# Optimization experiments

Measured on AMD Instinct MI355X. Metric: run time of the kernel, lower is better.

Reference implementation:

```python
import jax, jax.numpy as jnp
import numpy as np

N = 100000   # nodes
E = 500000   # edges
NS = 64      # scalar (0e) multiplicity
NV = 32      # vector (1o) multiplicity
DIM = NS + 3 * NV  # 160
AVG_NEI = 5.0
INV_SQRT3 = 0.5773502691896258


def setup_inputs() -> dict:
    key = jax.random.key(0)
    ks = jax.random.split(key, 14)
    return {
        "node_feats": jax.random.normal(ks[0], (N, DIM), jnp.float32),
        "node_attrs": jax.random.normal(ks[1], (N, 4), jnp.float32),
        "edge_message": jax.random.normal(ks[2], (E, DIM), jnp.float32),
        "edge_index": jax.random.randint(ks[3], (2, E), 0, N, dtype=jnp.int32),
        # UVU tensor product internal shared weights (one weight per u channel per path)
        "w_tp_00": jax.random.normal(ks[4], (NS,), jnp.float32),  # 0e x 0e -> 0e
        "w_tp_01": jax.random.normal(ks[5], (NS,), jnp.float32),  # 0e x 1o -> 1o
        "w_tp_10": jax.random.normal(ks[6], (NV,), jnp.float32),  # 1o x 0e -> 1o
        "w_tp_11": jax.random.normal(ks[7], (NV,), jnp.float32),  # 1o x 1o -> 0e
        # irreps Linear: tp out has 96x0e + 96x1o -> 96x0e + 32x1o
        "W_lin_s": jax.random.normal(ks[8], (NS + NV, NS + NV), jnp.float32),
        "W_lin_v": jax.random.normal(ks[9], (NS + NV, NV), jnp.float32),
        # FullyConnectedTensorProduct self-connection (uvw, v=1)
        "W_sc_000": jax.random.normal(ks[10], (NS, NS + NV), jnp.float32),
        "W_sc_110": jax.random.normal(ks[11], (NV, NS + NV), jnp.float32),
        "W_sc_011": jax.random.normal(ks[12], (NS, NV), jnp.float32),
        "W_sc_101": jax.random.normal(ks[13], (NV, NV), jnp.float32),
    }


def reference(node_feats, node_attrs, edge_message, edge_index,
              w_tp_00, w_tp_01, w_tp_10, w_tp_11,
              W_lin_s, W_lin_v, W_sc_000, W_sc_110, W_sc_011, W_sc_101):
    edge_dst = edge_index[1]
    # scatter-aggregate edge messages per destination node
    msg = jax.ops.segment_sum(edge_message, edge_dst, num_segments=N)
    msg = msg / jnp.sqrt(AVG_NEI)

    ms = msg[:, :NS]                         # [N, 64] scalars
    mv = msg[:, NS:].reshape(N, NV, 3)       # [N, 32, 3] vectors
    a_s = node_attrs[:, :1]                  # [N, 1]
    a_v = node_attrs[:, 1:]                  # [N, 3]

    # UVU tensor product (msg x attrs), per-channel shared weights
    s00 = ms * a_s * w_tp_00                                            # [N,64] 0e
    s11 = jnp.einsum('nuc,nc->nu', mv, a_v) * INV_SQRT3 * w_tp_11       # [N,32] 0e
    v01 = ms[:, :, None] * a_v[:, None, :] * w_tp_01[None, :, None]     # [N,64,3] 1o
    v10 = mv * a_s[:, :, None] * w_tp_10[None, :, None]                 # [N,32,3] 1o
    tp_s = jnp.concatenate([s00, s11], axis=1)   # [N,96]
    tp_v = jnp.concatenate([v01, v10], axis=1)   # [N,96,3]

    # irreps Linear (block diagonal per l, fan-in normalized)
    inv_fan = 1.0 / jnp.sqrt(jnp.float32(NS + NV))
    lin_s = (tp_s @ W_lin_s) * inv_fan                              # [N,96]
    lin_v = jnp.einsum('nuc,uw->nwc', tp_v, W_lin_v) * inv_fan      # [N,32,3]

    # self-connection: FullyConnectedTensorProduct(node_feats_in, node_attrs)
    xs = node_feats[:, :NS]
    xv = node_feats[:, NS:].reshape(N, NV, 3)
    inv2 = 1.0 / jnp.sqrt(2.0)
    sc_s = ((xs * a_s) @ W_sc_000 / jnp.sqrt(jnp.float32(NS))
            + (jnp.einsum('nuc,nc->nu', xv, a_v) * INV_SQRT3) @ W_sc_110 / jnp.sqrt(jnp.float32(NV))) * inv2
    sc_v = (jnp.einsum('nu,uw,nc->nwc', xs, W_sc_011, a_v) / jnp.sqrt(jnp.float32(NS))
            + jnp.einsum('nuc,uw->nwc', xv * a_s[:, :, None], W_sc_101) / jnp.sqrt(jnp.float32(NV))) * inv2

    h_s = lin_s + sc_s   # [N,96] = 64 scalars + 32 gates
    h_v = lin_v + sc_v   # [N,32,3]

    # gated activation: silu on scalars, sigmoid gates scale the vectors
    out_s = jax.nn.silu(h_s[:, :NS])
    gates = jax.nn.sigmoid(h_s[:, NS:])
    out_v = gates[:, :, None] * h_v
    return jnp.concatenate([out_s, out_v.reshape(N, NV * 3)], axis=1)  # [N,160]
```

## Files before the change

kernel.cpp:

```cpp
#include <hip/hip_runtime.h>

typedef unsigned short u16;
typedef unsigned int u32;

#define Nn 100000
#define Ee 500000
#define DIM 160
#define CAP 48

__device__ __forceinline__ float bf2f(u16 u) {
    return __uint_as_float(((u32)u) << 16);
}
__device__ __forceinline__ u16 f2bf(float f) {
    u32 i = __float_as_uint(f);
    return (u16)((i + 0x7FFFu + ((i >> 16) & 1u)) >> 16);
}

__global__ __launch_bounds__(256) void hist_fill_k(const int* __restrict__ ei,
                                                   int* __restrict__ cnt,
                                                   int* __restrict__ bucket) {
    int e = blockIdx.x * 256 + threadIdx.x;
    if (e >= Ee) return;
    int dst = ei[Ee + e];
    int pos = atomicAdd(&cnt[dst], 1);
    if (pos < CAP) bucket[(size_t)dst * CAP + pos] = e;
}

__global__ __launch_bounds__(256) void gather_tr_k(const float* __restrict__ em,
                                                   const int* __restrict__ bucket,
                                                   const int* __restrict__ cnt,
                                                   u16* __restrict__ msgT) {
    __shared__ u16 tile[160][66];
    int n0 = blockIdx.x * 64;
    int w = threadIdx.x >> 6;
    int lane = threadIdx.x & 63;
    const float s = 0.4472135954999579f;

    for (int i = 0; i < 16; ++i) {
        int n = n0 + w * 16 + i;
        float a0 = 0.f, a1 = 0.f, a2 = 0.f;
        if (n < Nn) {
            int deg = cnt[n];
            if (deg > CAP) deg = CAP;
            const int* base = bucket + (size_t)n * CAP;
            for (int k = 0; k < deg; ++k) {
                int e = base[k];
                const float* r = em + (size_t)e * DIM;
                a0 += r[lane];
                a1 += r[64 + lane];
                if (lane < 32) a2 += r[128 + lane];
            }
        }
        int col = w * 16 + i;
        tile[lane][col] = f2bf(a0 * s);
        tile[64 + lane][col] = f2bf(a1 * s);
        if (lane < 32) tile[128 + lane][col] = f2bf(a2 * s);
    }
    __syncthreads();
    for (int k = 0; k < 40; ++k) {
        int d = w * 40 + k;
        int n = n0 + lane;
        if (n < Nn) msgT[(size_t)d * Nn + n] = tile[d][lane];
    }
}

__global__ void transpose_f2b_k(const float* __restrict__ in, u16* __restrict__ outp) {
    __shared__ float t[32][33];
    int r0 = blockIdx.x * 32, c0 = blockIdx.y * 32;
    int tx = threadIdx.x, ty = threadIdx.y;
    t[ty][tx] = in[(size_t)(r0 + ty) * DIM + c0 + tx];
    __syncthreads();
    outp[(size_t)(c0 + ty) * Nn + r0 + tx] = f2bf(t[tx][ty]);
}

__global__ __launch_bounds__(256) void prep_weights_k(
    const float* __restrict__ Wls, const float* __restrict__ Wlv,
    const float* __restrict__ W000, const float* __restrict__ W110,
    const float* __restrict__ W011, const float* __restrict__ W101,
    const float* __restrict__ w00, const float* __restrict__ w01,
    const float* __restrict__ w10, const float* __restrict__ w11,
    float* __restrict__ W) {
    int i = blockIdx.x * 256 + threadIdx.x;
    const float inv_fan = 0.10206207261596577f;
    const float IS3 = 0.5773502691896258f;
    if (i < 9216) {
        int u = i / 96;
        float sc = inv_fan * (u < 64 ? w00[u] : IS3 * w11[u - 64]);
        W[i] = Wls[i] * sc;
    } else if (i < 12288) {
        int j = i - 9216; int u = j / 32;
        float sc = inv_fan * (u < 64 ? w01[u] : w10[u - 64]);
        W[i] = Wlv[j] * sc;
    } else if (i < 18432) {
        W[i] = W000[i - 12288] * 0.08838834764831845f;
    } else if (i < 21504) {
        W[i] = W110[i - 18432] * (0.125f * IS3);
    } else if (i < 23552) {
        W[i] = W011[i - 21504] * 0.08838834764831845f;
    } else {
        W[i] = W101[i - 23552] * 0.125f;
    }
}

__global__ __launch_bounds__(256) void node_s_k(
    const u16* __restrict__ msgT, const u16* __restrict__ featsT,
    const float* __restrict__ attrs, const float* __restrict__ W,
    float* __restrict__ out, float* __restrict__ gbuf) {
    __shared__ float st[256][33];
    int wb = blockIdx.y;
    int n0 = blockIdx.x * 256;
    int t = threadIdx.x;
    int n = n0 + t;
    bool active = (n < Nn);
    int nc = active ? n : (Nn - 1);

    const float* Wls  = W;
    const float* W000 = W + 12288;
    const float* W110 = W + 18432;

    float4 a = *reinterpret_cast<const float4*>(attrs + (size_t)nc * 4);
    float a_s = a.x, av0 = a.y, av1 = a.z, av2 = a.w;

    float accU[32], accJ[32];
    #pragma unroll
    for (int w = 0; w < 32; ++w) { accU[w] = 0.f; accJ[w] = 0.f; }

    const float* R1 = Wls + wb * 32;
    const float* R2 = W000 + wb * 32;
    const float* R3 = W110 + wb * 32;

    for (int u = 0; u < 64; ++u) {
        float m = bf2f(msgT[(size_t)u * Nn + nc]);
        float x = bf2f(featsT[(size_t)u * Nn + nc]);
        const float* r1 = R1 + u * 96;
        const float* r2 = R2 + u * 96;
        #pragma unroll
        for (int w = 0; w < 32; ++w) accU[w] += m * r1[w] + x * r2[w];
    }
    for (int j = 0; j < 32; ++j) {
        size_t d = (size_t)(64 + 3 * j) * Nn + nc;
        float dv = bf2f(msgT[d]) * av0 + bf2f(msgT[d + Nn]) * av1
                 + bf2f(msgT[d + 2 * Nn]) * av2;
        float dx = bf2f(featsT[d]) * av0 + bf2f(featsT[d + Nn]) * av1
                 + bf2f(featsT[d + 2 * Nn]) * av2;
        const float* r1 = R1 + (64 + j) * 96;
        const float* r2 = R3 + j * 96;
        #pragma unroll
        for (int w = 0; w < 32; ++w) accJ[w] += dv * r1[w] + dx * r2[w];
    }

    if (wb < 2) {
        #pragma unroll
        for (int w = 0; w < 32; ++w) {
            float h = a_s * accU[w] + accJ[w];
            st[t][w] = h / (1.f + __expf(-h));
        }
        __syncthreads();
        int off = wb * 32;
        for (int k = 0; k < 32; ++k) {
            int f = k * 256 + t;
            int node = f >> 5, w = f & 31;
            int n2 = n0 + node;
            if (n2 < Nn) out[(size_t)n2 * DIM + off + w] = st[node][w];
        }
    } else {
        #pragma unroll
        for (int w = 0; w < 32; ++w) {
            float h = a_s * accU[w] + accJ[w];
            if (active) gbuf[(size_t)w * Nn + n] = 1.f / (1.f + __expf(-h));
        }
    }
}

__global__ __launch_bounds__(256) void node_v_k(
    const u16* __restrict__ msgT, const u16* __restrict__ featsT,
    const float* __restrict__ attrs, const float* __restrict__ W,
    const float* __restrict__ gbuf, float* __restrict__ out) {
    __shared__ float st[256][49];
    int half = blockIdx.y;
    int w0 = half * 16;
    int n0 = blockIdx.x * 256;
    int t = threadIdx.x;
    int n = n0 + t;
    bool active = (n < Nn);
    int nc = active ? n : (Nn - 1);

    const float* Wlv  = W + 9216;
    const float* W011 = W + 21504;
    const float* W101 = W + 23552;

    float4 a = *reinterpret_cast<const float4*>(attrs + (size_t)nc * 4);
    float a_s = a.x;
    float av[3] = {a.y, a.z, a.w};

    float ss[16];
    #pragma unroll
    for (int w = 0; w < 16; ++w) ss[w] = 0.f;
    for (int u = 0; u < 64; ++u) {
        float m = bf2f(msgT[(size_t)u * Nn + nc]);
        float x = bf2f(featsT[(size_t)u * Nn + nc]);
        const float* r1 = Wlv + u * 32 + w0;
        const float* r2 = W011 + u * 32 + w0;
        #pragma unroll
        for (int w = 0; w < 16; ++w) ss[w] += m * r1[w] + x * r2[w];
    }

    float hj[16][3];
    #pragma unroll
    for (int w = 0; w < 16; ++w) {
        hj[w][0] = 0.f; hj[w][1] = 0.f; hj[w][2] = 0.f;
    }
    for (int j = 0; j < 32; ++j) {
        size_t d = (size_t)(64 + 3 * j) * Nn + nc;
        float m0 = bf2f(msgT[d]), m1 = bf2f(msgT[d + Nn]), m2 = bf2f(msgT[d + 2 * Nn]);
        float x0 = bf2f(featsT[d]), x1 = bf2f(featsT[d + Nn]), x2 = bf2f(featsT[d + 2 * Nn]);
        const float* r1 = Wlv + (64 + j) * 32 + w0;
        const float* r2 = W101 + j * 32 + w0;
        #pragma unroll
        for (int w = 0; w < 16; ++w) {
            float wv = r1[w], wx = r2[w];
            hj[w][0] += m0 * wv + x0 * wx;
            hj[w][1] += m1 * wv + x1 * wx;
            hj[w][2] += m2 * wv + x2 * wx;
        }
    }

    #pragma unroll
    for (int w = 0; w < 16; ++w) {
        float g = gbuf[(size_t)(w0 + w) * Nn + nc];
        #pragma unroll
        for (int c = 0; c < 3; ++c) {
            float hv = av[c] * ss[w] + a_s * hj[w][c];
            st[t][w * 3 + c] = g * hv;
        }
    }
    __syncthreads();
    int off = 64 + w0 * 3;
    for (int k = 0; k < 48; ++k) {
        int f = k * 256 + t;
        int node = f / 48;
        int idx = f - node * 48;
        int n2 = n0 + node;
        if (n2 < Nn) out[(size_t)n2 * DIM + off + idx] = st[node][idx];
    }
}

extern "C" void kernel_launch(void* const* d_in, const int* in_sizes, int n_in,
                              void* d_out, int out_size, void* d_ws, size_t ws_size,
                              hipStream_t stream) {
    const float* feats = (const float*)d_in[0];
    const float* attrs = (const float*)d_in[1];
    const float* em    = (const float*)d_in[2];
    const int*   ei    = (const int*)d_in[3];
    const float* w00   = (const float*)d_in[4];
    const float* w01   = (const float*)d_in[5];
    const float* w10   = (const float*)d_in[6];
    const float* w11   = (const float*)d_in[7];
    const float* Wls   = (const float*)d_in[8];
    const float* Wlv   = (const float*)d_in[9];
    const float* W000  = (const float*)d_in[10];
    const float* W110  = (const float*)d_in[11];
    const float* W011  = (const float*)d_in[12];
    const float* W101  = (const float*)d_in[13];

    char* ws = (char*)d_ws;
    int*   bucket = (int*)  (ws);
    int*   cnt    = (int*)  (ws + 19200000);
    u16*   msgT   = (u16*)  (ws + 19600000);
    u16*   featsT = (u16*)  (ws + 51600000);
    float* gbuf   = (float*)(ws + 83600000);
    float* W      = (float*)(ws + 96400000);

    hipMemsetAsync(cnt, 0, Nn * sizeof(int), stream);

    hist_fill_k<<<(Ee + 255) / 256, 256, 0, stream>>>(ei, cnt, bucket);

    gather_tr_k<<<(Nn + 63) / 64, 256, 0, stream>>>(em, bucket, cnt, msgT);

    dim3 tb(32, 32);
    transpose_f2b_k<<<dim3(Nn / 32, DIM / 32), tb, 0, stream>>>(feats, featsT);

    prep_weights_k<<<96, 256, 0, stream>>>(Wls, Wlv, W000, W110, W011, W101,
                                           w00, w01, w10, w11, W);

    node_s_k<<<dim3((Nn + 255) / 256, 3), 256, 0, stream>>>(msgT, featsT, attrs, W,
                                                            (float*)d_out, gbuf);

    node_v_k<<<dim3((Nn + 255) / 256, 2), 256, 0, stream>>>(msgT, featsT, attrs, W,
                                                            gbuf, (float*)d_out);
}
```

Before: 782.3 us.

## Fuse feats transpose into gather kernel and pack msg/feat bf16 pairs

Drops the separate node-feature transpose kernel and folds its work into the edge-gather kernel. That kernel now writes one interleaved u32 array holding the bf16 message in the high half and the bf16 feature in the low half. The node kernels then issue a single 32-bit load per channel instead of two 16-bit loads, and unpack with shifts and masks. The gather block grows to 512 threads with 8 nodes per wave, and 32-bit index arithmetic replaces size_t, at the cost of higher shared memory use per block.

```diff
diff --git a/kernel.cpp b/kernel.cpp
--- a/kernel.cpp
+++ b/kernel.cpp
@@ -8,9 +8,6 @@
 #define DIM 160
 #define CAP 48
 
-__device__ __forceinline__ float bf2f(u16 u) {
-    return __uint_as_float(((u32)u) << 16);
-}
 __device__ __forceinline__ u16 f2bf(float f) {
     u32 i = __float_as_uint(f);
     return (u16)((i + 0x7FFFu + ((i >> 16) & 1u)) >> 16);
@@ -26,19 +23,22 @@
     if (pos < CAP) bucket[(size_t)dst * CAP + pos] = e;
 }
 
-__global__ __launch_bounds__(256) void gather_tr_k(const float* __restrict__ em,
+__global__ __launch_bounds__(512) void gather_tr_k(const float* __restrict__ em,
+                                                   const float* __restrict__ feats,
                                                    const int* __restrict__ bucket,
                                                    const int* __restrict__ cnt,
-                                                   u16* __restrict__ msgT) {
-    __shared__ u16 tile[160][66];
+                                                   u32* __restrict__ mfT) {
+    __shared__ u32 tile[160][66];
     int n0 = blockIdx.x * 64;
     int w = threadIdx.x >> 6;
     int lane = threadIdx.x & 63;
     const float s = 0.4472135954999579f;
 
-    for (int i = 0; i < 16; ++i) {
-        int n = n0 + w * 16 + i;
+    for (int i = 0; i < 8; ++i) {
+        int col = w * 8 + i;
+        int n = n0 + col;
         float a0 = 0.f, a1 = 0.f, a2 = 0.f;
+        float f0 = 0.f, f1 = 0.f, f2 = 0.f;
         if (n < Nn) {
             int deg = cnt[n];
             if (deg > CAP) deg = CAP;
@@ -50,27 +50,24 @@
                 a1 += r[64 + lane];
                 if (lane < 32) a2 += r[128 + lane];
             }
-        }
-        int col = w * 16 + i;
-        tile[lane][col] = f2bf(a0 * s);
-        tile[64 + lane][col] = f2bf(a1 * s);
-        if (lane < 32) tile[128 + lane][col] = f2bf(a2 * s);
+            const float* f = feats + (size_t)n * DIM;
+            f0 = f[lane];
+            f1 = f[64 + lane];
+            if (lane < 32) f2 = f[128 + lane];
+        }
+        tile[lane][col]      = ((u32)f2bf(a0 * s) << 16) | f2bf(f0);
+        tile[64 + lane][col] = ((u32)f2bf(a1 * s) << 16) | f2bf(f1);
+        if (lane < 32)
+            tile[128 + lane][col] = ((u32)f2bf(a2 * s) << 16) | f2bf(f2);
     }
     __syncthreads();
-    for (int k = 0; k < 40; ++k) {
-        int d = w * 40 + k;
-        int n = n0 + lane;
-        if (n < Nn) msgT[(size_t)d * Nn + n] = tile[d][lane];
-    }
-}
-
-__global__ void transpose_f2b_k(const float* __restrict__ in, u16* __restrict__ outp) {
-    __shared__ float t[32][33];
-    int r0 = blockIdx.x * 32, c0 = blockIdx.y * 32;
-    int tx = threadIdx.x, ty = threadIdx.y;
-    t[ty][tx] = in[(size_t)(r0 + ty) * DIM + c0 + tx];
-    __syncthreads();
-    outp[(size_t)(c0 + ty) * Nn + r0 + tx] = f2bf(t[tx][ty]);
+    int n = n0 + lane;
+    if (n < Nn) {
+        for (int k = 0; k < 20; ++k) {
+            int d = w * 20 + k;
+            mfT[d * Nn + n] = tile[d][lane];
+        }
+    }
 }
 
 __global__ __launch_bounds__(256) void prep_weights_k(
@@ -102,10 +99,13 @@
     }
 }
 
+__device__ __forceinline__ float hi_f(u32 v) { return __uint_as_float(v & 0xFFFF0000u); }
+__device__ __forceinline__ float lo_f(u32 v) { return __uint_as_float(v << 16); }
+
 __global__ __launch_bounds__(256) void node_s_k(
-    const u16* __restrict__ msgT, const u16* __restrict__ featsT,
-    const float* __restrict__ attrs, const float* __restrict__ W,
-    float* __restrict__ out, float* __restrict__ gbuf) {
+    const u32* __restrict__ mfT, const float* __restrict__ attrs,
+    const float* __restrict__ W, float* __restrict__ out,
+    float* __restrict__ gbuf) {
     __shared__ float st[256][33];
     int wb = blockIdx.y;
     int n0 = blockIdx.x * 256;
@@ -130,19 +130,19 @@
     const float* R3 = W110 + wb * 32;
 
     for (int u = 0; u < 64; ++u) {
-        float m = bf2f(msgT[(size_t)u * Nn + nc]);
-        float x = bf2f(featsT[(size_t)u * Nn + nc]);
+        u32 v = mfT[u * Nn + nc];
+        float m = hi_f(v);
+        float x = lo_f(v);
         const float* r1 = R1 + u * 96;
         const float* r2 = R2 + u * 96;
         #pragma unroll
         for (int w = 0; w < 32; ++w) accU[w] += m * r1[w] + x * r2[w];
     }
     for (int j = 0; j < 32; ++j) {
-        size_t d = (size_t)(64 + 3 * j) * Nn + nc;
-        float dv = bf2f(msgT[d]) * av0 + bf2f(msgT[d + Nn]) * av1
-                 + bf2f(msgT[d + 2 * Nn]) * av2;
-        float dx = bf2f(featsT[d]) * av0 + bf2f(featsT[d + Nn]) * av1
-                 + bf2f(featsT[d + 2 * Nn]) * av2;
+        int d = (64 + 3 * j) * Nn + nc;
+        u32 v0 = mfT[d], v1 = mfT[d + Nn], v2 = mfT[d + 2 * Nn];
+        float dv = hi_f(v0) * av0 + hi_f(v1) * av1 + hi_f(v2) * av2;
+        float dx = lo_f(v0) * av0 + lo_f(v1) * av1 + lo_f(v2) * av2;
         const float* r1 = R1 + (64 + j) * 96;
         const float* r2 = R3 + j * 96;
         #pragma unroll
@@ -167,15 +167,15 @@
         #pragma unroll
         for (int w = 0; w < 32; ++w) {
             float h = a_s * accU[w] + accJ[w];
-            if (active) gbuf[(size_t)w * Nn + n] = 1.f / (1.f + __expf(-h));
+            if (active) gbuf[w * Nn + n] = 1.f / (1.f + __expf(-h));
         }
     }
 }
 
 __global__ __launch_bounds__(256) void node_v_k(
-    const u16* __restrict__ msgT, const u16* __restrict__ featsT,
-    const float* __restrict__ attrs, const float* __restrict__ W,
-    const float* __restrict__ gbuf, float* __restrict__ out) {
+    const u32* __restrict__ mfT, const float* __restrict__ attrs,
+    const float* __restrict__ W, const float* __restrict__ gbuf,
+    float* __restrict__ out) {
     __shared__ float st[256][49];
     int half = blockIdx.y;
     int w0 = half * 16;
@@ -197,8 +197,9 @@
     #pragma unroll
     for (int w = 0; w < 16; ++w) ss[w] = 0.f;
     for (int u = 0; u < 64; ++u) {
-        float m = bf2f(msgT[(size_t)u * Nn + nc]);
-        float x = bf2f(featsT[(size_t)u * Nn + nc]);
+        u32 v = mfT[u * Nn + nc];
+        float m = hi_f(v);
+        float x = lo_f(v);
         const float* r1 = Wlv + u * 32 + w0;
         const float* r2 = W011 + u * 32 + w0;
         #pragma unroll
@@ -211,9 +212,10 @@
         hj[w][0] = 0.f; hj[w][1] = 0.f; hj[w][2] = 0.f;
     }
     for (int j = 0; j < 32; ++j) {
-        size_t d = (size_t)(64 + 3 * j) * Nn + nc;
-        float m0 = bf2f(msgT[d]), m1 = bf2f(msgT[d + Nn]), m2 = bf2f(msgT[d + 2 * Nn]);
-        float x0 = bf2f(featsT[d]), x1 = bf2f(featsT[d + Nn]), x2 = bf2f(featsT[d + 2 * Nn]);
+        int d = (64 + 3 * j) * Nn + nc;
+        u32 v0 = mfT[d], v1 = mfT[d + Nn], v2 = mfT[d + 2 * Nn];
+        float m0 = hi_f(v0), m1 = hi_f(v1), m2 = hi_f(v2);
+        float x0 = lo_f(v0), x1 = lo_f(v1), x2 = lo_f(v2);
         const float* r1 = Wlv + (64 + j) * 32 + w0;
         const float* r2 = W101 + j * 32 + w0;
         #pragma unroll
@@ -227,7 +229,7 @@
 
     #pragma unroll
     for (int w = 0; w < 16; ++w) {
-        float g = gbuf[(size_t)(w0 + w) * Nn + nc];
+        float g = gbuf[(w0 + w) * Nn + nc];
         #pragma unroll
         for (int c = 0; c < 3; ++c) {
             float hv = av[c] * ss[w] + a_s * hj[w][c];
@@ -266,8 +268,7 @@
     char* ws = (char*)d_ws;
     int*   bucket = (int*)  (ws);
     int*   cnt    = (int*)  (ws + 19200000);
-    u16*   msgT   = (u16*)  (ws + 19600000);
-    u16*   featsT = (u16*)  (ws + 51600000);
+    u32*   mfT    = (u32*)  (ws + 19600000);
     float* gbuf   = (float*)(ws + 83600000);
     float* W      = (float*)(ws + 96400000);
 
@@ -275,17 +276,14 @@
 
     hist_fill_k<<<(Ee + 255) / 256, 256, 0, stream>>>(ei, cnt, bucket);
 
-    gather_tr_k<<<(Nn + 63) / 64, 256, 0, stream>>>(em, bucket, cnt, msgT);
-
-    dim3 tb(32, 32);
-    transpose_f2b_k<<<dim3(Nn / 32, DIM / 32), tb, 0, stream>>>(feats, featsT);
+    gather_tr_k<<<(Nn + 63) / 64, 512, 0, stream>>>(em, feats, bucket, cnt, mfT);
 
     prep_weights_k<<<96, 256, 0, stream>>>(Wls, Wlv, W000, W110, W011, W101,
                                            w00, w01, w10, w11, W);
 
-    node_s_k<<<dim3((Nn + 255) / 256, 3), 256, 0, stream>>>(msgT, featsT, attrs, W,
+    node_s_k<<<dim3((Nn + 255) / 256, 3), 256, 0, stream>>>(mfT, attrs, W,
                                                             (float*)d_out, gbuf);
 
-    node_v_k<<<dim3((Nn + 255) / 256, 2), 256, 0, stream>>>(msgT, featsT, attrs, W,
+    node_v_k<<<dim3((Nn + 255) / 256, 2), 256, 0, stream>>>(mfT, attrs, W,
                                                             gbuf, (float*)d_out);
 }
```

Measured after the change: 801.1 us. 2.4% more time.
